# Performance work log

Measured on AMD Instinct MI355X. Metric: run time of the kernel, lower is better.

The kernel has to match this reference:

```python
import jax, jax.numpy as jnp
import numpy as np

N = 50000      # nodes
F_IN = 256     # nfeat
HID = 64       # nhid (per-head, layer 1)
H = 4          # heads layer 1
OUT = 64       # nhid2 (layer 2, heads=1, concat=False)
E = 800000     # edges (self-loops appended in reference)
NEG_SLOPE = 0.2  # PyG GATConv default LeakyReLU slope


def setup_inputs() -> dict:
    key = jax.random.key(0)
    ks = jax.random.split(key, 10)
    x = jax.random.normal(ks[0], (N, F_IN), dtype=jnp.float32)
    adj = jax.random.randint(ks[1], (2, E), 0, N)
    s1 = 1.0 / np.sqrt(F_IN)
    s2 = 1.0 / np.sqrt(H * HID)
    W1 = (jax.random.normal(ks[2], (F_IN, H * HID), dtype=jnp.float32) * s1)
    att_src1 = jax.random.normal(ks[3], (H, HID), dtype=jnp.float32) * 0.1
    att_dst1 = jax.random.normal(ks[4], (H, HID), dtype=jnp.float32) * 0.1
    b1 = jnp.zeros((H * HID,), dtype=jnp.float32)
    W2 = (jax.random.normal(ks[5], (H * HID, OUT), dtype=jnp.float32) * s2)
    att_src2 = jax.random.normal(ks[6], (1, OUT), dtype=jnp.float32) * 0.1
    att_dst2 = jax.random.normal(ks[7], (1, OUT), dtype=jnp.float32) * 0.1
    b2 = jnp.zeros((OUT,), dtype=jnp.float32)
    return {"x": x, "adj": adj, "W1": W1, "att_src1": att_src1,
            "att_dst1": att_dst1, "b1": b1, "W2": W2, "att_src2": att_src2,
            "att_dst2": att_dst2, "b2": b2}


def _gat_conv(x, src, dst, W, a_src, a_dst, bias, heads, out_ch, concat):
    n = x.shape[0]
    h = (x @ W).reshape(n, heads, out_ch)                    # [N, H, C]
    alpha_src = jnp.einsum('nhc,hc->nh', h, a_src)           # [N, H]
    alpha_dst = jnp.einsum('nhc,hc->nh', h, a_dst)           # [N, H]
    alpha = jax.nn.leaky_relu(alpha_src[src] + alpha_dst[dst],
                              negative_slope=NEG_SLOPE)      # [E, H]
    # segment softmax over incoming edges of each dst node
    m = jax.ops.segment_max(alpha, dst, num_segments=n)      # [N, H]
    e = jnp.exp(alpha - m[dst])
    denom = jax.ops.segment_sum(e, dst, num_segments=n)      # [N, H]
    a = e / denom[dst]                                       # [E, H]
    msg = h[src] * a[:, :, None]                             # [E, H, C]
    out = jax.ops.segment_sum(msg, dst, num_segments=n)      # [N, H, C]
    if concat:
        out = out.reshape(n, heads * out_ch)
    else:
        out = out.mean(axis=1)
    return out + bias


def reference(x, adj, W1, att_src1, att_dst1, b1, W2, att_src2, att_dst2, b2):
    loops = jnp.arange(N, dtype=adj.dtype)
    src = jnp.concatenate([adj[0], loops])
    dst = jnp.concatenate([adj[1], loops])
    h = _gat_conv(x, src, dst, W1, att_src1, att_dst1, b1, H, HID, True)
    h = jax.nn.elu(h)
    out = _gat_conv(h, src, dst, W2, att_src2, att_dst2, b2, 1, OUT, False)
    return jax.nn.log_softmax(out, axis=1)
```

## Files before the change

### kernel.cpp

```cpp
#include <hip/hip_runtime.h>
#include <cstdint>
#include <cstddef>

#define NN    50000
#define EE    800000
#define SLOPE 0.2f
#define MT64  782
#define CAP   64

#define NBIN  391
#define PBLK  512
#define EPB   1563
#define BCAP  16
#define OCAP  8192

typedef unsigned short ushortT;
typedef __attribute__((ext_vector_type(8))) short short8;
typedef __attribute__((ext_vector_type(4))) float floatx4;

__device__ __forceinline__ float lrelu(float x){ return x > 0.f ? x : SLOPE * x; }
__device__ __forceinline__ float eluf(float x){ return x > 0.f ? x : __expf(x) - 1.f; }
__device__ __forceinline__ ushortT f2b(float f){ unsigned u = __float_as_uint(f); u += 0x7fff + ((u >> 16) & 1); return (ushortT)(u >> 16); }
__device__ __forceinline__ float   b2f(ushortT b){ return __uint_as_float(((unsigned)b) << 16); }

__global__ __launch_bounds__(256) void binCast_k(const int* __restrict__ srcA,
                                                 const int* __restrict__ dstA,
                                                 unsigned* __restrict__ binned,
                                                 ushortT* __restrict__ cnt2,
                                                 unsigned* __restrict__ ovf,
                                                 int* __restrict__ ovfcnt,
                                                 const float* __restrict__ W1,
                                                 const float* __restrict__ W2,
                                                 ushortT* __restrict__ W1T,
                                                 ushortT* __restrict__ W2T)
{
    __shared__ int      hist[NBIN];
    __shared__ unsigned lrec[NBIN][BCAP];
    if (blockIdx.x >= PBLK) {
        int k = blockIdx.x - PBLK, t = threadIdx.x;
        W1T[t * 256 + k] = f2b(W1[k * 256 + t]);
        if (t < 64) W2T[t * 256 + k] = f2b(W2[k * 64 + t]);
        return;
    }
    const int blk = blockIdx.x;
    const int tid = threadIdx.x;
    for (int i = tid; i < NBIN; i += 256) hist[i] = 0;
    __syncthreads();

    const int e0 = blk * EPB;
    const int e1 = min(e0 + EPB, EE);
    for (int e = e0 + tid; e < e1; e += 256) {
        int s = srcA[e], d = dstA[e];
        int bin = d >> 7;
        unsigned rec = ((unsigned)s << 7) | (unsigned)(d & 127);
        int r = atomicAdd(&hist[bin], 1);
        if (r < BCAP) lrec[bin][r] = rec;
        else {
            int o = atomicAdd(ovfcnt, 1);
            if (o < OCAP) ovf[o] = ((unsigned)s << 16) | (unsigned)d;
        }
    }
    __syncthreads();

    for (int b = tid; b < NBIN; b += 256)
        cnt2[(size_t)blk * NBIN + b] = (ushortT)min(hist[b], BCAP);
    for (int sIdx = tid; sIdx < NBIN * BCAP; sIdx += 256) {
        int b = sIdx / BCAP;
        int i = sIdx - b * BCAP;
        if (i < min(hist[b], BCAP))
            binned[((size_t)b * PBLK + blk) * BCAP + i] = lrec[b][i];
    }
}

__global__ __launch_bounds__(256, 3) void gemm1_k(const float* __restrict__ x,
                                                  const ushortT* __restrict__ W1T,
                                                  const float* __restrict__ attS,
                                                  const float* __restrict__ attD,
                                                  ushortT* __restrict__ h1b,
                                                  float* __restrict__ asrc,
                                                  float* __restrict__ adst)
{
    const int tid  = threadIdx.x;
    const int w    = tid >> 6;
    const int lane = tid & 63;
    const int m16  = lane & 15;
    const int quad = lane >> 4;
    const int wr   = w >> 1;
    const int wc   = w & 1;
    const int rowbase = blockIdx.x * 64 + wr * 32;
    const int colbase = wc * 128;

    const long r0 = min(rowbase + m16,      NN - 1);
    const long r1 = min(rowbase + 16 + m16, NN - 1);
    const float* a0p = x + r0 * 256 + quad * 8;
    const float* a1p = x + r1 * 256 + quad * 8;
    const ushortT* bp0 = W1T + (size_t)(colbase + m16) * 256 + quad * 8;

    floatx4 acc[2][8];
    #pragma unroll
    for (int i = 0; i < 2; ++i)
        #pragma unroll
        for (int j = 0; j < 8; ++j) acc[i][j] = (floatx4){0.f, 0.f, 0.f, 0.f};

    #pragma unroll
    for (int it = 0; it < 8; ++it) {
        const int k0 = it * 32;
        float4 fa00 = *(const float4*)(a0p + k0);
        float4 fa01 = *(const float4*)(a0p + k0 + 4);
        float4 fa10 = *(const float4*)(a1p + k0);
        float4 fa11 = *(const float4*)(a1p + k0 + 4);
        uint4 fb[8];
        #pragma unroll
        for (int j = 0; j < 8; ++j)
            fb[j] = *(const uint4*)(bp0 + (size_t)j * 16 * 256 + k0);

        ushortT a16[16];
        a16[0]=f2b(fa00.x); a16[1]=f2b(fa00.y); a16[2]=f2b(fa00.z); a16[3]=f2b(fa00.w);
        a16[4]=f2b(fa01.x); a16[5]=f2b(fa01.y); a16[6]=f2b(fa01.z); a16[7]=f2b(fa01.w);
        a16[8]=f2b(fa10.x); a16[9]=f2b(fa10.y); a16[10]=f2b(fa10.z); a16[11]=f2b(fa10.w);
        a16[12]=f2b(fa11.x); a16[13]=f2b(fa11.y); a16[14]=f2b(fa11.z); a16[15]=f2b(fa11.w);
        short8 af0 = *(short8*)(a16);
        short8 af1 = *(short8*)(a16 + 8);

        #pragma unroll
        for (int j = 0; j < 8; ++j) {
            short8 bf = *(short8*)(&fb[j]);
            acc[0][j] = __builtin_amdgcn_mfma_f32_16x16x32_bf16(af0, bf, acc[0][j], 0, 0, 0);
            acc[1][j] = __builtin_amdgcn_mfma_f32_16x16x32_bf16(af1, bf, acc[1][j], 0, 0, 0);
        }
    }

    float attSv[8], attDv[8];
    #pragma unroll
    for (int j = 0; j < 8; ++j) {
        attSv[j] = attS[colbase + j * 16 + m16];
        attDv[j] = attD[colbase + j * 16 + m16];
    }

    #pragma unroll
    for (int i = 0; i < 2; ++i) {
        #pragma unroll
        for (int r = 0; r < 4; ++r) {
            int row = rowbase + i * 16 + quad * 4 + r;
            bool ok = row < NN;
            if (ok) {
                #pragma unroll
                for (int j = 0; j < 8; ++j)
                    h1b[(size_t)row * 256 + colbase + j * 16 + m16] = f2b(acc[i][j][r]);
            }
            float d0 = 0.f, d1 = 0.f, e0 = 0.f, e1 = 0.f;
            #pragma unroll
            for (int jj = 0; jj < 4; ++jj) {
                d0 += acc[i][jj][r]     * attSv[jj];
                e0 += acc[i][jj][r]     * attDv[jj];
                d1 += acc[i][jj + 4][r] * attSv[jj + 4];
                e1 += acc[i][jj + 4][r] * attDv[jj + 4];
            }
            #pragma unroll
            for (int off = 1; off < 16; off <<= 1) {
                d0 += __shfl_xor(d0, off); e0 += __shfl_xor(e0, off);
                d1 += __shfl_xor(d1, off); e1 += __shfl_xor(e1, off);
            }
            if (ok && m16 == 0) {
                int hb = row * 4 + wc * 2;
                asrc[hb] = d0; asrc[hb + 1] = d1;
                adst[hb] = e0; adst[hb + 1] = e1;
            }
        }
    }
}

__global__ __launch_bounds__(256) void bucket_k(const unsigned* __restrict__ binned,
                                                const ushortT* __restrict__ cnt2,
                                                const unsigned* __restrict__ ovf,
                                                const int* __restrict__ ovfcnt,
                                                ushortT* __restrict__ esorted,
                                                int* __restrict__ cnt)
{
    __shared__ ushortT c2[PBLK];
    __shared__ int     lcnt[128];
    __shared__ ushortT lbuck[128][CAP];
    const int b = blockIdx.x;
    const int tid = threadIdx.x;

    for (int i = tid; i < 128; i += 256) lcnt[i] = 0;
    for (int i = tid; i < PBLK; i += 256) c2[i] = cnt2[(size_t)i * NBIN + b];
    __syncthreads();

    for (int s0 = tid; s0 < PBLK * BCAP; s0 += 1024) {
        unsigned recs[4]; int ok[4];
        #pragma unroll
        for (int q = 0; q < 4; ++q) {
            int s = s0 + q * 256;
            int blk = s / BCAP;
            int i = s - blk * BCAP;
            ok[q] = (i < (int)c2[blk]);
            recs[q] = ok[q] ? binned[((size_t)b * PBLK + blk) * BCAP + i] : 0u;
        }
        #pragma unroll
        for (int q = 0; q < 4; ++q) {
            if (ok[q]) {
                int dl = recs[q] & 127;
                int r = atomicAdd(&lcnt[dl], 1);
                if (r < CAP) lbuck[dl][r] = (ushortT)(recs[q] >> 7);
            }
        }
    }

    int nov = *ovfcnt;
    nov = nov > OCAP ? OCAP : nov;
    for (int i = tid; i < nov; i += 256) {
        unsigned rec = ovf[i];
        int d = rec & 0xFFFF;
        if ((d >> 7) == b) {
            int r = atomicAdd(&lcnt[d & 127], 1);
            if (r < CAP) lbuck[d & 127][r] = (ushortT)(rec >> 16);
        }
    }
    __syncthreads();

    const int nbase = b << 7;
    if (tid < 128) {
        int n = nbase + tid;
        if (n < NN) cnt[n] = lcnt[tid];
    }
    unsigned* ed = (unsigned*)(esorted + (size_t)nbase * CAP);
    const unsigned* ls = (const unsigned*)(&lbuck[0][0]);
    for (int i = tid; i < 128 * (CAP / 2); i += 256) {
        if (nbase + (i >> 5) < NN) ed[i] = ls[i];
    }
}

__global__ __launch_bounds__(256) void gemm2_k(const ushortT* __restrict__ a2b,
                                               const ushortT* __restrict__ W2T,
                                               const float* __restrict__ attS,
                                               const float* __restrict__ attD,
                                               ushortT* __restrict__ t2b,
                                               float* __restrict__ asrc,
                                               float* __restrict__ adst)
{
    const int tid  = threadIdx.x;
    const int w    = tid >> 6;
    const int lane = tid & 63;
    const int m16  = lane & 15;
    const int quad = lane >> 4;
    const int rowbase = blockIdx.x * 64 + w * 16;

    const long r0 = min(rowbase + m16, NN - 1);
    const ushortT* ap  = a2b + r0 * 256 + quad * 8;
    const ushortT* bp0 = W2T + (size_t)m16 * 256 + quad * 8;

    floatx4 acc[4];
    #pragma unroll
    for (int j = 0; j < 4; ++j) acc[j] = (floatx4){0.f, 0.f, 0.f, 0.f};

    #pragma unroll
    for (int it = 0; it < 8; ++it) {
        const int k0 = it * 32;
        uint4 fa = *(const uint4*)(ap + k0);
        uint4 fb[4];
        #pragma unroll
        for (int j = 0; j < 4; ++j)
            fb[j] = *(const uint4*)(bp0 + (size_t)j * 16 * 256 + k0);
        short8 af = *(short8*)(&fa);
        #pragma unroll
        for (int j = 0; j < 4; ++j) {
            short8 bf = *(short8*)(&fb[j]);
            acc[j] = __builtin_amdgcn_mfma_f32_16x16x32_bf16(af, bf, acc[j], 0, 0, 0);
        }
    }

    float attSv[4], attDv[4];
    #pragma unroll
    for (int j = 0; j < 4; ++j) {
        attSv[j] = attS[j * 16 + m16];
        attDv[j] = attD[j * 16 + m16];
    }

    #pragma unroll
    for (int r = 0; r < 4; ++r) {
        int row = rowbase + quad * 4 + r;
        bool ok = row < NN;
        if (ok) {
            #pragma unroll
            for (int j = 0; j < 4; ++j)
                t2b[(size_t)row * 64 + j * 16 + m16] = f2b(acc[j][r]);
        }
        float ds = 0.f, dd = 0.f;
        #pragma unroll
        for (int j = 0; j < 4; ++j) {
            ds += acc[j][r] * attSv[j];
            dd += acc[j][r] * attDv[j];
        }
        #pragma unroll
        for (int off = 1; off < 16; off <<= 1) {
            ds += __shfl_xor(ds, off);
            dd += __shfl_xor(dd, off);
        }
        if (ok && m16 == 0) {
            asrc[row] = ds;
            adst[row] = dd;
        }
    }
}

__global__ __launch_bounds__(256) void agg1_k(const ushortT* __restrict__ esorted,
                                              const int* __restrict__ cnt,
                                              const ushortT* __restrict__ h1b,
                                              const float* __restrict__ asrc,
                                              const float* __restrict__ adst,
                                              const float* __restrict__ b1,
                                              ushortT* __restrict__ a2b)
{
    __shared__ float pbuf[4][64][4];
    __shared__ int   sbuf[4][64];
    int w = threadIdx.x >> 6;
    int lane = threadIdx.x & 63;
    int n = blockIdx.x * 4 + w;
    if (n >= NN) return;
    int start = n * CAP;
    int deg = min(max(cnt[n], 0), CAP);
    float4 adv = *(const float4*)(adst + (size_t)n * 4);
    float4 asf = *(const float4*)(asrc + (size_t)n * 4);
    int h = lane >> 4;
    int c4 = lane * 4;

    float4 pself;
    pself.x = __expf(lrelu(asf.x + adv.x));
    pself.y = __expf(lrelu(asf.y + adv.y));
    pself.z = __expf(lrelu(asf.z + adv.z));
    pself.w = __expf(lrelu(asf.w + adv.w));
    float psh = (h < 2) ? (h == 0 ? pself.x : pself.y) : (h == 2 ? pself.z : pself.w);

    ushort4 hsv = *(const ushort4*)(h1b + (size_t)n * 256 + c4);
    float4 ac0 = make_float4(b2f(hsv.x) * psh, b2f(hsv.y) * psh, b2f(hsv.z) * psh, b2f(hsv.w) * psh);
    float4 ac1 = make_float4(0.f,0.f,0.f,0.f);
    float4 ac2 = make_float4(0.f,0.f,0.f,0.f);
    float4 ac3 = make_float4(0.f,0.f,0.f,0.f);
    float4 ssv = make_float4(0.f, 0.f, 0.f, 0.f);

    if (lane < deg) {
        int s = esorted[start + lane];
        float4 a = *(const float4*)(asrc + (size_t)s * 4);
        float4 pv;
        pv.x = __expf(lrelu(a.x + adv.x));
        pv.y = __expf(lrelu(a.y + adv.y));
        pv.z = __expf(lrelu(a.z + adv.z));
        pv.w = __expf(lrelu(a.w + adv.w));
        ssv = pv;
        *(float4*)(&pbuf[w][lane][0]) = pv;
        sbuf[w][lane] = s;
    } else {
        *(float4*)(&pbuf[w][lane][0]) = make_float4(0.f, 0.f, 0.f, 0.f);
        sbuf[w][lane] = 0;
    }
    __builtin_amdgcn_wave_barrier();

    int nb = (deg + 7) >> 3;
    ushort4 bufA[8], bufB[8];

#define LOADR(BUF, J0) { _Pragma("unroll") for (int q = 0; q < 8; ++q) { \
        int sq = sbuf[w][(J0) + q]; \
        BUF[q] = *(const ushort4*)(h1b + (size_t)sq * 256 + c4); } }
#define CONSR(BUF, J0) { _Pragma("unroll") for (int q = 0; q < 8; ++q) { \
        float p = pbuf[w][(J0) + q][h]; \
        float4* ac = (q & 3) == 0 ? &ac0 : (q & 3) == 1 ? &ac1 : (q & 3) == 2 ? &ac2 : &ac3; \
        ac->x += b2f(BUF[q].x) * p; ac->y += b2f(BUF[q].y) * p; \
        ac->z += b2f(BUF[q].z) * p; ac->w += b2f(BUF[q].w) * p; } }

    if (nb > 0) {
        LOADR(bufA, 0)
        #pragma unroll
        for (int b = 0; b < 8; ++b) {
            const int j0 = b << 3;
            if (b & 1) {
                if (b + 1 < nb) LOADR(bufA, j0 + 8)
                CONSR(bufB, j0)
            } else {
                if (b + 1 < nb) LOADR(bufB, j0 + 8)
                CONSR(bufA, j0)
            }
            if (b + 1 >= nb) break;
        }
    }
#undef LOADR
#undef CONSR

    #pragma unroll
    for (int off = 1; off < 64; off <<= 1) {
        ssv.x += __shfl_xor(ssv.x, off); ssv.y += __shfl_xor(ssv.y, off);
        ssv.z += __shfl_xor(ssv.z, off); ssv.w += __shfl_xor(ssv.w, off);
    }
    float ssh = (h < 2) ? (h == 0 ? ssv.x : ssv.y) : (h == 2 ? ssv.z : ssv.w);
    float rdh = 1.f / (ssh + psh);

    float4 bv = *(const float4*)(b1 + c4);
    ushort4 o;
    o.x = f2b(eluf((ac0.x + ac1.x + ac2.x + ac3.x) * rdh + bv.x));
    o.y = f2b(eluf((ac0.y + ac1.y + ac2.y + ac3.y) * rdh + bv.y));
    o.z = f2b(eluf((ac0.z + ac1.z + ac2.z + ac3.z) * rdh + bv.z));
    o.w = f2b(eluf((ac0.w + ac1.w + ac2.w + ac3.w) * rdh + bv.w));
    *(ushort4*)(a2b + (size_t)n * 256 + c4) = o;
}

__global__ __launch_bounds__(256) void agg2_k(const ushortT* __restrict__ esorted,
                                              const int* __restrict__ cnt,
                                              const ushortT* __restrict__ t2b,
                                              const float* __restrict__ asrc,
                                              const float* __restrict__ adst,
                                              const float* __restrict__ b2,
                                              float* __restrict__ out)
{
    __shared__ float pbuf[4][64];
    __shared__ int   sbuf[4][64];
    int w = threadIdx.x >> 6;
    int lane = threadIdx.x & 63;
    int n = blockIdx.x * 4 + w;
    if (n >= NN) return;
    int start = n * CAP;
    int deg = min(max(cnt[n], 0), CAP);
    float adv = adst[n];

    float pself = __expf(lrelu(asrc[n] + adv));
    float a0 = b2f(t2b[(size_t)n * 64 + lane]) * pself;
    float a1 = 0.f, a2 = 0.f, a3 = 0.f;
    float ss = 0.f;

    if (lane < deg) {
        int s = esorted[start + lane];
        float p = __expf(lrelu(asrc[s] + adv));
        ss = p;
        pbuf[w][lane] = p;
        sbuf[w][lane] = s;
    } else {
        pbuf[w][lane] = 0.f;
        sbuf[w][lane] = 0;
    }
    __builtin_amdgcn_wave_barrier();

    int nb = (deg + 7) >> 3;
    ushortT bufA[8], bufB[8];

#define LOADR2(BUF, J0) { _Pragma("unroll") for (int q = 0; q < 8; ++q) { \
        int sq = sbuf[w][(J0) + q]; \
        BUF[q] = t2b[(size_t)sq * 64 + lane]; } }
#define CONSR2(BUF, J0) { _Pragma("unroll") for (int q = 0; q < 8; ++q) { \
        float p = pbuf[w][(J0) + q]; \
        float* ac = (q & 3) == 0 ? &a0 : (q & 3) == 1 ? &a1 : (q & 3) == 2 ? &a2 : &a3; \
        *ac += b2f(BUF[q]) * p; } }

    if (nb > 0) {
        LOADR2(bufA, 0)
        #pragma unroll
        for (int b = 0; b < 8; ++b) {
            const int j0 = b << 3;
            if (b & 1) {
                if (b + 1 < nb) LOADR2(bufA, j0 + 8)
                CONSR2(bufB, j0)
            } else {
                if (b + 1 < nb) LOADR2(bufB, j0 + 8)
                CONSR2(bufA, j0)
            }
            if (b + 1 >= nb) break;
        }
    }
#undef LOADR2
#undef CONSR2

    #pragma unroll
    for (int off = 1; off < 64; off <<= 1) ss += __shfl_xor(ss, off);
    float v = (a0 + a1 + a2 + a3) / (ss + pself) + b2[lane];

    float m2 = v;
    #pragma unroll
    for (int off = 32; off; off >>= 1) m2 = fmaxf(m2, __shfl_xor(m2, off));
    float ex = __expf(v - m2);
    float sm = ex;
    #pragma unroll
    for (int off = 32; off; off >>= 1) sm += __shfl_xor(sm, off);
    out[(size_t)n * 64 + lane] = v - m2 - __logf(sm);
}

extern "C" void kernel_launch(void* const* d_in, const int* in_sizes, int n_in,
                              void* d_out, int out_size, void* d_ws, size_t ws_size,
                              hipStream_t stream)
{
    const float* x   = (const float*)d_in[0];
    const int*   adj = (const int*)  d_in[1];
    const float* W1  = (const float*)d_in[2];
    const float* as1 = (const float*)d_in[3];
    const float* ad1 = (const float*)d_in[4];
    const float* b1  = (const float*)d_in[5];
    const float* W2  = (const float*)d_in[6];
    const float* as2 = (const float*)d_in[7];
    const float* ad2 = (const float*)d_in[8];
    const float* b2  = (const float*)d_in[9];
    float* out = (float*)d_out;

    const size_t szH1b = (size_t)NN * 256 * 2;
    const size_t szT2b = (size_t)NN * 64 * 2;
    const size_t szA4  = (size_t)NN * 4 * 4;
    const size_t szA1  = (size_t)NN * 4;
    const size_t szE   = (size_t)NN * CAP * 2;
    const size_t szBin = (size_t)NBIN * PBLK * BCAP * 4;
    const size_t szC2  = (size_t)PBLK * NBIN * 2;

    char* p = (char*)d_ws;
    ushortT* h1b  = (ushortT*)p; p += szH1b;
    ushortT* a2b  = (ushortT*)p; p += szH1b;
    ushortT* t2b  = (ushortT*)p; p += szT2b;
    ushortT* W1T  = (ushortT*)p; p += 256 * 256 * 2;
    ushortT* W2T  = (ushortT*)p; p += 64 * 256 * 2;
    float* asrc1  = (float*)p; p += szA4;
    float* adst1  = (float*)p; p += szA4;
    float* asrc2  = (float*)p; p += szA1;
    float* adst2  = (float*)p; p += szA1;
    ushortT* esorted = (ushortT*)p; p += szE;
    int* cnt      = (int*)p; p += szA1;
    unsigned* binned = (unsigned*)p; p += szBin;
    ushortT* cnt2 = (ushortT*)p; p += szC2;
    unsigned* ovf = (unsigned*)p; p += (size_t)OCAP * 4;
    int* ovfcnt   = (int*)p; p += 64;

    const int nwb = (NN + 3) / 4;

    hipMemsetAsync(ovfcnt, 0, sizeof(int), stream);

    binCast_k<<<PBLK + 256, 256, 0, stream>>>(adj, adj + EE, binned, cnt2, ovf, ovfcnt,
                                              W1, W2, W1T, W2T);

    bucket_k<<<NBIN, 256, 0, stream>>>(binned, cnt2, ovf, ovfcnt, esorted, cnt);

    gemm1_k<<<MT64, 256, 0, stream>>>(x, W1T, as1, ad1, h1b, asrc1, adst1);

    agg1_k<<<nwb, 256, 0, stream>>>(esorted, cnt, h1b, asrc1, adst1, b1, a2b);
    gemm2_k<<<MT64, 256, 0, stream>>>(a2b, W2T, as2, ad2, t2b, asrc2, adst2);
    agg2_k<<<nwb, 256, 0, stream>>>(esorted, cnt, t2b, asrc2, adst2, b2, out);
}
```

Baseline: 279.6 us.

## Fuse edge binning into GEMM1 launch and widen dst bins to 256 nodes

```diff
diff --git a/kernel.cpp b/kernel.cpp
--- a/kernel.cpp
+++ b/kernel.cpp
@@ -8,10 +8,11 @@
 #define MT64  782
 #define CAP   64
 
-#define NBIN  391
+#define NBIN  196
+#define DSH   8
 #define PBLK  512
 #define EPB   1563
-#define BCAP  16
+#define BCAP  20
 #define OCAP  8192
 
 typedef unsigned short ushortT;
@@ -23,63 +24,63 @@
 __device__ __forceinline__ ushortT f2b(float f){ unsigned u = __float_as_uint(f); u += 0x7fff + ((u >> 16) & 1); return (ushortT)(u >> 16); }
 __device__ __forceinline__ float   b2f(ushortT b){ return __uint_as_float(((unsigned)b) << 16); }
 
-__global__ __launch_bounds__(256) void binCast_k(const int* __restrict__ srcA,
-                                                 const int* __restrict__ dstA,
-                                                 unsigned* __restrict__ binned,
-                                                 ushortT* __restrict__ cnt2,
-                                                 unsigned* __restrict__ ovf,
-                                                 int* __restrict__ ovfcnt,
-                                                 const float* __restrict__ W1,
-                                                 const float* __restrict__ W2,
-                                                 ushortT* __restrict__ W1T,
-                                                 ushortT* __restrict__ W2T)
+__global__ __launch_bounds__(256) void castW_k(const float* __restrict__ W1, const float* __restrict__ W2,
+                                               ushortT* __restrict__ W1T, ushortT* __restrict__ W2T)
+{
+    int k = blockIdx.x, t = threadIdx.x;
+    W1T[t * 256 + k] = f2b(W1[k * 256 + t]);
+    if (t < 64) W2T[t * 256 + k] = f2b(W2[k * 64 + t]);
+}
+
+__global__ __launch_bounds__(256, 3) void gemmbin_k(const float* __restrict__ x,
+                                                    const ushortT* __restrict__ W1T,
+                                                    const float* __restrict__ attS,
+                                                    const float* __restrict__ attD,
+                                                    ushortT* __restrict__ h1b,
+                                                    float* __restrict__ asrc,
+                                                    float* __restrict__ adst,
+                                                    const int* __restrict__ srcA,
+                                                    const int* __restrict__ dstA,
+                                                    unsigned* __restrict__ binned,
+                                                    ushortT* __restrict__ cnt2,
+                                                    unsigned* __restrict__ ovf,
+                                                    int* __restrict__ ovfcnt)
 {
     __shared__ int      hist[NBIN];
     __shared__ unsigned lrec[NBIN][BCAP];
-    if (blockIdx.x >= PBLK) {
-        int k = blockIdx.x - PBLK, t = threadIdx.x;
-        W1T[t * 256 + k] = f2b(W1[k * 256 + t]);
-        if (t < 64) W2T[t * 256 + k] = f2b(W2[k * 64 + t]);
+
+    if (blockIdx.x >= MT64) {
+        const int blk = blockIdx.x - MT64;
+        const int tid = threadIdx.x;
+        for (int i = tid; i < NBIN; i += 256) hist[i] = 0;
+        __syncthreads();
+
+        const int e0 = blk * EPB;
+        const int e1 = min(e0 + EPB, EE);
+        for (int e = e0 + tid; e < e1; e += 256) {
+            int s = srcA[e], d = dstA[e];
+            int bin = d >> DSH;
+            unsigned rec = ((unsigned)s << DSH) | (unsigned)(d & 255);
+            int r = atomicAdd(&hist[bin], 1);
+            if (r < BCAP) lrec[bin][r] = rec;
+            else {
+                int o = atomicAdd(ovfcnt, 1);
+                if (o < OCAP) ovf[o] = ((unsigned)s << 16) | (unsigned)d;
+            }
+        }
+        __syncthreads();
+
+        for (int b = tid; b < NBIN; b += 256)
+            cnt2[(size_t)blk * NBIN + b] = (ushortT)min(hist[b], BCAP);
+        for (int sIdx = tid; sIdx < NBIN * BCAP; sIdx += 256) {
+            int b = sIdx / BCAP;
+            int i = sIdx - b * BCAP;
+            if (i < min(hist[b], BCAP))
+                binned[((size_t)b * PBLK + blk) * BCAP + i] = lrec[b][i];
+        }
         return;
     }
-    const int blk = blockIdx.x;
-    const int tid = threadIdx.x;
-    for (int i = tid; i < NBIN; i += 256) hist[i] = 0;
-    __syncthreads();
-
-    const int e0 = blk * EPB;
-    const int e1 = min(e0 + EPB, EE);
-    for (int e = e0 + tid; e < e1; e += 256) {
-        int s = srcA[e], d = dstA[e];
-        int bin = d >> 7;
-        unsigned rec = ((unsigned)s << 7) | (unsigned)(d & 127);
-        int r = atomicAdd(&hist[bin], 1);
-        if (r < BCAP) lrec[bin][r] = rec;
-        else {
-            int o = atomicAdd(ovfcnt, 1);
-            if (o < OCAP) ovf[o] = ((unsigned)s << 16) | (unsigned)d;
-        }
-    }
-    __syncthreads();
-
-    for (int b = tid; b < NBIN; b += 256)
-        cnt2[(size_t)blk * NBIN + b] = (ushortT)min(hist[b], BCAP);
-    for (int sIdx = tid; sIdx < NBIN * BCAP; sIdx += 256) {
-        int b = sIdx / BCAP;
-        int i = sIdx - b * BCAP;
-        if (i < min(hist[b], BCAP))
-            binned[((size_t)b * PBLK + blk) * BCAP + i] = lrec[b][i];
-    }
-}
-
-__global__ __launch_bounds__(256, 3) void gemm1_k(const float* __restrict__ x,
-                                                  const ushortT* __restrict__ W1T,
-                                                  const float* __restrict__ attS,
-                                                  const float* __restrict__ attD,
-                                                  ushortT* __restrict__ h1b,
-                                                  float* __restrict__ asrc,
-                                                  float* __restrict__ adst)
-{
+
     const int tid  = threadIdx.x;
     const int w    = tid >> 6;
     const int lane = tid & 63;
@@ -178,12 +179,12 @@
                                                 int* __restrict__ cnt)
 {
     __shared__ ushortT c2[PBLK];
-    __shared__ int     lcnt[128];
-    __shared__ ushortT lbuck[128][CAP];
+    __shared__ int     lcnt[256];
+    __shared__ ushortT lbuck[256][CAP];
     const int b = blockIdx.x;
     const int tid = threadIdx.x;
 
-    for (int i = tid; i < 128; i += 256) lcnt[i] = 0;
+    lcnt[tid] = 0;
     for (int i = tid; i < PBLK; i += 256) c2[i] = cnt2[(size_t)i * NBIN + b];
     __syncthreads();
 
@@ -200,9 +201,9 @@
         #pragma unroll
         for (int q = 0; q < 4; ++q) {
             if (ok[q]) {
-                int dl = recs[q] & 127;
+                int dl = recs[q] & 255;
                 int r = atomicAdd(&lcnt[dl], 1);
-                if (r < CAP) lbuck[dl][r] = (ushortT)(recs[q] >> 7);
+                if (r < CAP) lbuck[dl][r] = (ushortT)(recs[q] >> DSH);
             }
         }
     }
@@ -212,21 +213,21 @@
     for (int i = tid; i < nov; i += 256) {
         unsigned rec = ovf[i];
         int d = rec & 0xFFFF;
-        if ((d >> 7) == b) {
-            int r = atomicAdd(&lcnt[d & 127], 1);
-            if (r < CAP) lbuck[d & 127][r] = (ushortT)(rec >> 16);
+        if ((d >> DSH) == b) {
+            int r = atomicAdd(&lcnt[d & 255], 1);
+            if (r < CAP) lbuck[d & 255][r] = (ushortT)(rec >> 16);
         }
     }
     __syncthreads();
 
-    const int nbase = b << 7;
-    if (tid < 128) {
+    const int nbase = b << DSH;
+    {
         int n = nbase + tid;
         if (n < NN) cnt[n] = lcnt[tid];
     }
     unsigned* ed = (unsigned*)(esorted + (size_t)nbase * CAP);
     const unsigned* ls = (const unsigned*)(&lbuck[0][0]);
-    for (int i = tid; i < 128 * (CAP / 2); i += 256) {
+    for (int i = tid; i < 256 * (CAP / 2); i += 256) {
         if (nbase + (i >> 5) < NN) ed[i] = ls[i];
     }
 }
@@ -526,12 +527,12 @@
 
     hipMemsetAsync(ovfcnt, 0, sizeof(int), stream);
 
-    binCast_k<<<PBLK + 256, 256, 0, stream>>>(adj, adj + EE, binned, cnt2, ovf, ovfcnt,
-                                              W1, W2, W1T, W2T);
+    castW_k<<<256, 256, 0, stream>>>(W1, W2, W1T, W2T);
+
+    gemmbin_k<<<MT64 + PBLK, 256, 0, stream>>>(x, W1T, as1, ad1, h1b, asrc1, adst1,
+                                               adj, adj + EE, binned, cnt2, ovf, ovfcnt);
 
     bucket_k<<<NBIN, 256, 0, stream>>>(binned, cnt2, ovf, ovfcnt, esorted, cnt);
-
-    gemm1_k<<<MT64, 256, 0, stream>>>(x, W1T, as1, ad1, h1b, asrc1, adst1);
 
     agg1_k<<<nwb, 256, 0, stream>>>(esorted, cnt, h1b, asrc1, adst1, b1, a2b);
     gemm2_k<<<MT64, 256, 0, stream>>>(a2b, W2T, as2, ad2, t2b, asrc2, adst2);
```

Result: no change. 281.3 us (+0.6%).
